# Performance work log

Hardware: AMD Instinct MI355X
Metric: run time of the kernel (lower is better)

## Reference

```python
import jax, jax.numpy as jnp
import numpy as np

T, D_IN, D_OUT, E = 8192, 1024, 1024, 8
LN_EPS = 1e-5


def setup_inputs() -> dict:
    key = jax.random.key(0)
    k1, k2, k3 = jax.random.split(key, 3)
    x = jax.random.normal(k1, (T, D_IN), dtype=jnp.float32)
    # tokens are pre-sorted by expert; equal load => capacity = T // E per expert
    expert_frequency = jnp.full((E,), T // E, dtype=jnp.int64)
    # per-expert Linear(input_dim, output_dim) params
    W = jax.random.normal(k2, (E, D_IN, D_OUT), dtype=jnp.float32) / np.sqrt(D_IN)
    b = jax.random.normal(k3, (E, D_OUT), dtype=jnp.float32) * 0.02
    # per-expert LayerNorm(output_dim) affine params
    ln_gamma = jnp.ones((E, D_OUT), dtype=jnp.float32)
    ln_beta = jnp.zeros((E, D_OUT), dtype=jnp.float32)
    return {
        "expert_ordered_input": x,
        "expert_frequency": expert_frequency,
        "W": W,
        "b": b,
        "ln_gamma": ln_gamma,
        "ln_beta": ln_beta,
    }


def reference(expert_ordered_input, expert_frequency, W, b, ln_gamma, ln_beta):
    # Grouped-GEMM form of: split tokens by expert_frequency, apply per-expert
    # LayerBlock (Linear -> relu -> LayerNorm), then concat along token dim.
    # Frequencies are equal (capacity = T // E), so the ragged split is a reshape.
    x = expert_ordered_input
    n_tok, d_in = x.shape
    n_exp = W.shape[0]
    cap = n_tok // n_exp  # static capacity per expert
    xe = x.reshape(n_exp, cap, d_in)                       # [E, cap, d_in]
    h = jnp.einsum("ecd,edf->ecf", xe, W) + b[:, None, :]  # [E, cap, d_out]
    h = jax.nn.relu(h)
    mu = jnp.mean(h, axis=-1, keepdims=True)
    var = jnp.var(h, axis=-1, keepdims=True)
    hn = (h - mu) * jax.lax.rsqrt(var + LN_EPS)
    out = hn * ln_gamma[:, None, :] + ln_beta[:, None, :]
    return out.reshape(n_tok, -1)                          # concat over experts
```

## Files before the change

kernel.cpp:

```cpp
#include <hip/hip_runtime.h>
#include <hip/hip_bf16.h>
#include <stdint.h>

#define T_TOK 8192
#define DIN   1024
#define DOUT  1024
#define NEXP  8
#define CAP   1024
#define LN_EPS 1e-5f

#define BM 128
#define BN 128
#define BK 32

typedef __attribute__((ext_vector_type(8))) short short8;
typedef __attribute__((ext_vector_type(4))) float f32x4;

__device__ __forceinline__ unsigned short f2bf(float f) {
    union { float f; unsigned int u; } v; v.f = f;
    unsigned int u = v.u;
    unsigned int r = u + 0x7FFFu + ((u >> 16) & 1u);
    return (unsigned short)(r >> 16);
}
__device__ __forceinline__ float bf2f(unsigned short h) {
    union { unsigned int u; float f; } v; v.u = ((unsigned int)h) << 16;
    return v.f;
}

__device__ __forceinline__ void gld16(void* l, const void* g) {
    __builtin_amdgcn_global_load_lds(
        (const __attribute__((address_space(1))) unsigned int*)(uintptr_t)g,
        (__attribute__((address_space(3))) unsigned int*)(uintptr_t)l,
        16, 0, 0);
}

__global__ __launch_bounds__(256) void prep_kernel(
    const float* __restrict__ X, const float* __restrict__ W,
    unsigned short* __restrict__ Xb, unsigned short* __restrict__ Wt) {
    __shared__ float tile[32][33];
    int blk = blockIdx.x;
    int tid = threadIdx.x;
    if (blk < 8192) {
        int e = blk & 7;
        int r = blk >> 3;
        size_t i = ((size_t)(e * CAP + r)) * 256 + tid;
        float4 v = ((const float4*)X)[i];
        ushort4 o;
        o.x = f2bf(v.x); o.y = f2bf(v.y); o.z = f2bf(v.z); o.w = f2bf(v.w);
        ((ushort4*)Xb)[i] = o;
    } else {
        int t  = blk - 8192;
        int e  = t & 7;
        int tl = t >> 3;
        int k0 = (tl >> 5) * 32;
        int n0 = (tl & 31) * 32;
        const float* Wp = W + (size_t)e * DIN * DOUT;
        unsigned short* Wtp = Wt + (size_t)e * DIN * DOUT;
        {
            int k  = tid >> 3;
            int c4 = tid & 7;
            float4 v = *(const float4*)(Wp + (size_t)(k0 + k) * DOUT + n0 + c4 * 4);
            tile[k][c4 * 4 + 0] = v.x; tile[k][c4 * 4 + 1] = v.y;
            tile[k][c4 * 4 + 2] = v.z; tile[k][c4 * 4 + 3] = v.w;
        }
        __syncthreads();
        {
            int n  = tid >> 3;
            int kc = tid & 7;
            ushort4 o;
            o.x = f2bf(tile[kc * 4 + 0][n]);
            o.y = f2bf(tile[kc * 4 + 1][n]);
            o.z = f2bf(tile[kc * 4 + 2][n]);
            o.w = f2bf(tile[kc * 4 + 3][n]);
            *(ushort4*)(Wtp + (size_t)(n0 + n) * DIN + k0 + kc * 4) = o;
        }
    }
}

__global__ __launch_bounds__(256, 2) void gemm5_kernel(
    const unsigned short* __restrict__ Xb,
    const unsigned short* __restrict__ Wt,
    const float* __restrict__ Bias,
    unsigned short* __restrict__ Hb,
    float2* __restrict__ P)
{
    __shared__ unsigned short As[4][BM * BK];
    __shared__ unsigned short Bs[4][BN * BK];

    int blk = blockIdx.x;
    int e   = blk & 7;
    int mi  = blk >> 6;
    int m0  = mi * BM;
    int ni  = (blk >> 3) & 7;
    int n0  = ni * BN;

    int tid  = threadIdx.x;
    int wave = tid >> 6;
    int lane = tid & 63;
    int wm   = (wave >> 1) * 64;
    int wn   = (wave & 1) * 64;
    int lrow = lane & 15;
    int quad = lane >> 4;

    const unsigned short* Ag = Xb + (size_t)(e * CAP + m0) * DIN;
    const unsigned short* Bg = Wt + (size_t)e * DOUT * DIN + (size_t)n0 * DIN;

    int l0 = tid;
    int l1 = tid + 256;
    int ar0 = l0 >> 2, ac0 = (l0 & 3) * 8;
    int ar1 = l1 >> 2, ac1 = (l1 & 3) * 8;

    f32x4 acc[4][4];
#pragma unroll
    for (int i = 0; i < 4; i++)
#pragma unroll
        for (int j = 0; j < 4; j++)
            acc[i][j] = (f32x4)(0.0f);

    for (int kb = 0; kb < DIN; kb += 4 * BK) {
#pragma unroll
        for (int s = 0; s < 4; s++) {
            int k0 = kb + s * BK;
            gld16(&As[s][l0 * 8], Ag + (size_t)ar0 * DIN + k0 + ac0);
            gld16(&As[s][l1 * 8], Ag + (size_t)ar1 * DIN + k0 + ac1);
            gld16(&Bs[s][l0 * 8], Bg + (size_t)ar0 * DIN + k0 + ac0);
            gld16(&Bs[s][l1 * 8], Bg + (size_t)ar1 * DIN + k0 + ac1);
        }
        __syncthreads();

#pragma unroll
        for (int s = 0; s < 4; s++) {
            short8 af[4], bf[4];
#pragma unroll
            for (int i = 0; i < 4; i++)
                af[i] = *(const short8*)&As[s][(wm + i * 16 + lrow) * BK + quad * 8];
#pragma unroll
            for (int j = 0; j < 4; j++)
                bf[j] = *(const short8*)&Bs[s][(wn + j * 16 + lrow) * BK + quad * 8];
#pragma unroll
            for (int i = 0; i < 4; i++)
#pragma unroll
                for (int j = 0; j < 4; j++)
                    acc[i][j] = __builtin_amdgcn_mfma_f32_16x16x32_bf16(af[i], bf[j], acc[i][j], 0, 0, 0);
        }
        __syncthreads();
    }

    float bias[4];
#pragma unroll
    for (int j = 0; j < 4; j++)
        bias[j] = Bias[e * DOUT + n0 + wn + j * 16 + lrow];

    int tok0  = e * CAP + m0 + wm;
    int chunk = ni * 2 + (wave & 1);

#pragma unroll
    for (int i = 0; i < 4; i++) {
#pragma unroll
        for (int r = 0; r < 4; r++) {
            float s = 0.f, ss = 0.f;
#pragma unroll
            for (int j = 0; j < 4; j++) {
                float v = fmaxf(acc[i][j][r] + bias[j], 0.f);
                acc[i][j][r] = v;
                s += v;
                ss = fmaf(v, v, ss);
            }
#pragma unroll
            for (int m = 1; m <= 8; m <<= 1) {
                s  += __shfl_xor(s, m);
                ss += __shfl_xor(ss, m);
            }
            int grow = tok0 + i * 16 + quad * 4 + r;
            if (lrow == 0)
                P[(size_t)grow * 16 + chunk] = make_float2(s, ss);
#pragma unroll
            for (int j = 0; j < 4; j++) {
                int gcol = n0 + wn + j * 16 + lrow;
                Hb[(size_t)grow * DOUT + gcol] = f2bf(acc[i][j][r]);
            }
        }
    }
}

__global__ __launch_bounds__(256) void ln2_kernel(
    const unsigned short* __restrict__ Hb,
    const float2* __restrict__ P,
    const float* __restrict__ G,
    const float* __restrict__ Bt,
    float* __restrict__ Out)
{
    int blk = blockIdx.x;
    int e   = blk & 7;
    int row = e * CAP + (blk >> 3);
    int tid = threadIdx.x;
    __shared__ float sh[2];

    if (tid < 16) {
        float2 p = P[(size_t)row * 16 + tid];
        float s = p.x, ss = p.y;
#pragma unroll
        for (int m = 1; m <= 8; m <<= 1) {
            s  += __shfl_xor(s, m);
            ss += __shfl_xor(ss, m);
        }
        if (tid == 0) {
            float mu  = s * (1.0f / DOUT);
            float var = fmaxf(ss * (1.0f / DOUT) - mu * mu, 0.f);
            sh[0] = mu;
            sh[1] = rsqrtf(var + LN_EPS);
        }
    }
    __syncthreads();
    float mu = sh[0], rs = sh[1];

    ushort4 hb = ((const ushort4*)Hb)[(size_t)row * 256 + tid];
    float4 g = ((const float4*)G)[e * 256 + tid];
    float4 b = ((const float4*)Bt)[e * 256 + tid];
    float4 y;
    y.x = (bf2f(hb.x) - mu) * rs * g.x + b.x;
    y.y = (bf2f(hb.y) - mu) * rs * g.y + b.y;
    y.z = (bf2f(hb.z) - mu) * rs * g.z + b.z;
    y.w = (bf2f(hb.w) - mu) * rs * g.w + b.w;
    ((float4*)Out)[(size_t)row * 256 + tid] = y;
}

extern "C" void kernel_launch(void* const* d_in, const int* in_sizes, int n_in,
                              void* d_out, int out_size, void* d_ws, size_t ws_size,
                              hipStream_t stream) {
    const float* x  = (const float*)d_in[0];
    const float* W  = (const float*)d_in[2];
    const float* b  = (const float*)d_in[3];
    const float* g  = (const float*)d_in[4];
    const float* be = (const float*)d_in[5];
    float* out = (float*)d_out;

    const size_t WT_BYTES = (size_t)NEXP * DIN * DOUT * 2;
    const size_t XB_BYTES = (size_t)T_TOK * DIN * 2;
    const size_t P_BYTES  = (size_t)T_TOK * 16 * 8;
    const size_t HB_BYTES = (size_t)T_TOK * DOUT * 2;
    if (ws_size < WT_BYTES + XB_BYTES + P_BYTES + HB_BYTES) return;

    unsigned short* Wt = (unsigned short*)d_ws;
    unsigned short* Xb = (unsigned short*)((char*)d_ws + WT_BYTES);
    float2* P = (float2*)((char*)d_ws + WT_BYTES + XB_BYTES);
    unsigned short* Hb = (unsigned short*)((char*)d_ws + WT_BYTES + XB_BYTES + P_BYTES);

    dim3 tb(256);
    prep_kernel<<<dim3(16384), tb, 0, stream>>>(x, W, Xb, Wt);
    gemm5_kernel<<<dim3(512), tb, 0, stream>>>(Xb, Wt, b, Hb, P);
    ln2_kernel<<<dim3(8192), tb, 0, stream>>>(Hb, P, g, be, out);
}
```

Baseline: 153.8 us.

## Double-buffer GEMM K-loop and coarsen prep and layernorm blocks

The GEMM main loop now uses two LDS buffers of 64-wide K chunks. It issues global-to-LDS loads for the next chunk while computing MFMAs on the current one, so memory latency is hidden instead of stalling behind a barrier. The prep kernel processes four rows of X and a 64x64 transposed W tile per block, and the layernorm kernel handles two rows per block. Both changes reduce block count and per-block overhead. The GEMM keeps the same total LDS footprint, and the coarser blocks lower parallelism in the memory-bound kernels.

```diff
diff --git a/kernel.cpp b/kernel.cpp
--- a/kernel.cpp
+++ b/kernel.cpp
@@ -37,55 +37,63 @@
 __global__ __launch_bounds__(256) void prep_kernel(
     const float* __restrict__ X, const float* __restrict__ W,
     unsigned short* __restrict__ Xb, unsigned short* __restrict__ Wt) {
-    __shared__ float tile[32][33];
+    __shared__ float tile[64][65];
     int blk = blockIdx.x;
     int tid = threadIdx.x;
-    if (blk < 8192) {
-        int e = blk & 7;
-        int r = blk >> 3;
-        size_t i = ((size_t)(e * CAP + r)) * 256 + tid;
-        float4 v = ((const float4*)X)[i];
-        ushort4 o;
-        o.x = f2bf(v.x); o.y = f2bf(v.y); o.z = f2bf(v.z); o.w = f2bf(v.w);
-        ((ushort4*)Xb)[i] = o;
+    if (blk < 2048) {
+        int e  = blk & 7;
+        int r0 = (blk >> 3) * 4;
+        size_t base = ((size_t)(e * CAP + r0)) * 256 + tid;
+#pragma unroll
+        for (int q = 0; q < 4; q++) {
+            size_t i = base + (size_t)q * 256;
+            float4 v = ((const float4*)X)[i];
+            ushort4 o;
+            o.x = f2bf(v.x); o.y = f2bf(v.y); o.z = f2bf(v.z); o.w = f2bf(v.w);
+            ((ushort4*)Xb)[i] = o;
+        }
     } else {
-        int t  = blk - 8192;
+        int t  = blk - 2048;
         int e  = t & 7;
         int tl = t >> 3;
-        int k0 = (tl >> 5) * 32;
-        int n0 = (tl & 31) * 32;
+        int k0 = (tl >> 4) * 64;
+        int n0 = (tl & 15) * 64;
         const float* Wp = W + (size_t)e * DIN * DOUT;
         unsigned short* Wtp = Wt + (size_t)e * DIN * DOUT;
-        {
-            int k  = tid >> 3;
-            int c4 = tid & 7;
-            float4 v = *(const float4*)(Wp + (size_t)(k0 + k) * DOUT + n0 + c4 * 4);
-            tile[k][c4 * 4 + 0] = v.x; tile[k][c4 * 4 + 1] = v.y;
-            tile[k][c4 * 4 + 2] = v.z; tile[k][c4 * 4 + 3] = v.w;
+        int rr = tid >> 4;
+        int cc = tid & 15;
+#pragma unroll
+        for (int q = 0; q < 4; q++) {
+            int k = rr + q * 16;
+            float4 v = *(const float4*)(Wp + (size_t)(k0 + k) * DOUT + n0 + cc * 4);
+            tile[k][cc * 4 + 0] = v.x;
+            tile[k][cc * 4 + 1] = v.y;
+            tile[k][cc * 4 + 2] = v.z;
+            tile[k][cc * 4 + 3] = v.w;
         }
         __syncthreads();
-        {
-            int n  = tid >> 3;
-            int kc = tid & 7;
+#pragma unroll
+        for (int q = 0; q < 4; q++) {
+            int n = rr + q * 16;
             ushort4 o;
-            o.x = f2bf(tile[kc * 4 + 0][n]);
-            o.y = f2bf(tile[kc * 4 + 1][n]);
-            o.z = f2bf(tile[kc * 4 + 2][n]);
-            o.w = f2bf(tile[kc * 4 + 3][n]);
-            *(ushort4*)(Wtp + (size_t)(n0 + n) * DIN + k0 + kc * 4) = o;
-        }
-    }
-}
-
-__global__ __launch_bounds__(256, 2) void gemm5_kernel(
+            o.x = f2bf(tile[cc * 4 + 0][n]);
+            o.y = f2bf(tile[cc * 4 + 1][n]);
+            o.z = f2bf(tile[cc * 4 + 2][n]);
+            o.w = f2bf(tile[cc * 4 + 3][n]);
+            *(ushort4*)(Wtp + (size_t)(n0 + n) * DIN + k0 + cc * 4) = o;
+        }
+    }
+}
+
+__global__ __launch_bounds__(256, 2) void gemm6_kernel(
     const unsigned short* __restrict__ Xb,
     const unsigned short* __restrict__ Wt,
     const float* __restrict__ Bias,
     unsigned short* __restrict__ Hb,
     float2* __restrict__ P)
 {
-    __shared__ unsigned short As[4][BM * BK];
-    __shared__ unsigned short Bs[4][BN * BK];
+    __shared__ unsigned short As[2][2][BM * BK];
+    __shared__ unsigned short Bs[2][2][BN * BK];
 
     int blk = blockIdx.x;
     int e   = blk & 7;
@@ -117,34 +125,54 @@
         for (int j = 0; j < 4; j++)
             acc[i][j] = (f32x4)(0.0f);
 
-    for (int kb = 0; kb < DIN; kb += 4 * BK) {
-#pragma unroll
-        for (int s = 0; s < 4; s++) {
-            int k0 = kb + s * BK;
-            gld16(&As[s][l0 * 8], Ag + (size_t)ar0 * DIN + k0 + ac0);
-            gld16(&As[s][l1 * 8], Ag + (size_t)ar1 * DIN + k0 + ac1);
-            gld16(&Bs[s][l0 * 8], Bg + (size_t)ar0 * DIN + k0 + ac0);
-            gld16(&Bs[s][l1 * 8], Bg + (size_t)ar1 * DIN + k0 + ac1);
-        }
+#define STAGE(buf, kb)                                                        \
+    {                                                                         \
+        _Pragma("unroll")                                                     \
+        for (int s = 0; s < 2; s++) {                                         \
+            int k0 = (kb) + s * BK;                                           \
+            gld16(&As[buf][s][l0 * 8], Ag + (size_t)ar0 * DIN + k0 + ac0);    \
+            gld16(&As[buf][s][l1 * 8], Ag + (size_t)ar1 * DIN + k0 + ac1);    \
+            gld16(&Bs[buf][s][l0 * 8], Bg + (size_t)ar0 * DIN + k0 + ac0);    \
+            gld16(&Bs[buf][s][l1 * 8], Bg + (size_t)ar1 * DIN + k0 + ac1);    \
+        }                                                                     \
+    }
+
+#define COMPUTE(buf)                                                          \
+    {                                                                         \
+        _Pragma("unroll")                                                     \
+        for (int s = 0; s < 2; s++) {                                         \
+            short8 af[4], bfr[4];                                             \
+            _Pragma("unroll")                                                 \
+            for (int i = 0; i < 4; i++)                                       \
+                af[i] = *(const short8*)&As[buf][s][(wm + i * 16 + lrow) * BK + quad * 8]; \
+            _Pragma("unroll")                                                 \
+            for (int j = 0; j < 4; j++)                                       \
+                bfr[j] = *(const short8*)&Bs[buf][s][(wn + j * 16 + lrow) * BK + quad * 8]; \
+            _Pragma("unroll")                                                 \
+            for (int i = 0; i < 4; i++)                                       \
+                _Pragma("unroll")                                             \
+                for (int j = 0; j < 4; j++)                                   \
+                    acc[i][j] = __builtin_amdgcn_mfma_f32_16x16x32_bf16(af[i], bfr[j], acc[i][j], 0, 0, 0); \
+        }                                                                     \
+    }
+
+    STAGE(0, 0);
+    __syncthreads();
+    for (int kb = 64; kb < 960; kb += 128) {
+        STAGE(1, kb);
+        COMPUTE(0);
         __syncthreads();
-
-#pragma unroll
-        for (int s = 0; s < 4; s++) {
-            short8 af[4], bf[4];
-#pragma unroll
-            for (int i = 0; i < 4; i++)
-                af[i] = *(const short8*)&As[s][(wm + i * 16 + lrow) * BK + quad * 8];
-#pragma unroll
-            for (int j = 0; j < 4; j++)
-                bf[j] = *(const short8*)&Bs[s][(wn + j * 16 + lrow) * BK + quad * 8];
-#pragma unroll
-            for (int i = 0; i < 4; i++)
-#pragma unroll
-                for (int j = 0; j < 4; j++)
-                    acc[i][j] = __builtin_amdgcn_mfma_f32_16x16x32_bf16(af[i], bf[j], acc[i][j], 0, 0, 0);
-        }
+        STAGE(0, kb + 64);
+        COMPUTE(1);
         __syncthreads();
     }
+    STAGE(1, 960);
+    COMPUTE(0);
+    __syncthreads();
+    COMPUTE(1);
+
+#undef STAGE
+#undef COMPUTE
 
     float bias[4];
 #pragma unroll
@@ -192,37 +220,42 @@
 {
     int blk = blockIdx.x;
     int e   = blk & 7;
-    int row = e * CAP + (blk >> 3);
+    int r2  = (blk >> 3) * 2;
+    int row0 = e * CAP + r2;
     int tid = threadIdx.x;
-    __shared__ float sh[2];
-
-    if (tid < 16) {
-        float2 p = P[(size_t)row * 16 + tid];
+    __shared__ float sh[2][2];
+
+    if (tid < 32) {
+        int r = tid >> 4;
+        float2 p = P[(size_t)(row0 + r) * 16 + (tid & 15)];
         float s = p.x, ss = p.y;
 #pragma unroll
         for (int m = 1; m <= 8; m <<= 1) {
             s  += __shfl_xor(s, m);
             ss += __shfl_xor(ss, m);
         }
-        if (tid == 0) {
+        if ((tid & 15) == 0) {
             float mu  = s * (1.0f / DOUT);
             float var = fmaxf(ss * (1.0f / DOUT) - mu * mu, 0.f);
-            sh[0] = mu;
-            sh[1] = rsqrtf(var + LN_EPS);
+            sh[r][0] = mu;
+            sh[r][1] = rsqrtf(var + LN_EPS);
         }
     }
     __syncthreads();
-    float mu = sh[0], rs = sh[1];
-
-    ushort4 hb = ((const ushort4*)Hb)[(size_t)row * 256 + tid];
+
     float4 g = ((const float4*)G)[e * 256 + tid];
     float4 b = ((const float4*)Bt)[e * 256 + tid];
-    float4 y;
-    y.x = (bf2f(hb.x) - mu) * rs * g.x + b.x;
-    y.y = (bf2f(hb.y) - mu) * rs * g.y + b.y;
-    y.z = (bf2f(hb.z) - mu) * rs * g.z + b.z;
-    y.w = (bf2f(hb.w) - mu) * rs * g.w + b.w;
-    ((float4*)Out)[(size_t)row * 256 + tid] = y;
+#pragma unroll
+    for (int r = 0; r < 2; r++) {
+        float mu = sh[r][0], rs = sh[r][1];
+        ushort4 hb = ((const ushort4*)Hb)[(size_t)(row0 + r) * 256 + tid];
+        float4 y;
+        y.x = (bf2f(hb.x) - mu) * rs * g.x + b.x;
+        y.y = (bf2f(hb.y) - mu) * rs * g.y + b.y;
+        y.z = (bf2f(hb.z) - mu) * rs * g.z + b.z;
+        y.w = (bf2f(hb.w) - mu) * rs * g.w + b.w;
+        ((float4*)Out)[(size_t)(row0 + r) * 256 + tid] = y;
+    }
 }
 
 extern "C" void kernel_launch(void* const* d_in, const int* in_sizes, int n_in,
@@ -247,7 +280,7 @@
     unsigned short* Hb = (unsigned short*)((char*)d_ws + WT_BYTES + XB_BYTES + P_BYTES);
 
     dim3 tb(256);
-    prep_kernel<<<dim3(16384), tb, 0, stream>>>(x, W, Xb, Wt);
-    gemm5_kernel<<<dim3(512), tb, 0, stream>>>(Xb, Wt, b, Hb, P);
-    ln2_kernel<<<dim3(8192), tb, 0, stream>>>(Hb, P, g, be, out);
-}
+    prep_kernel<<<dim3(4096), tb, 0, stream>>>(x, W, Xb, Wt);
+    gemm6_kernel<<<dim3(512), tb, 0, stream>>>(Xb, Wt, b, Hb, P);
+    ln2_kernel<<<dim3(4096), tb, 0, stream>>>(Hb, P, g, be, out);
+}
```

New measurement: 147.3 us. -4.3%, faster.
